# Kernel optimization log

Measured on AMD Instinct MI355X. Metric: run time of the kernel, lower is better.

The kernel has to match this reference:

```python
import jax, jax.numpy as jnp
import numpy as np

NEG_INF = -1e30
LRELU_SLOPE = 0.01
KEEP_SCALE = 2.0  # 1/(1-p) with p=0.5


def mixed_act(x, tid):
    # x: [B, H], tid: [H] int type ids
    # 0 relu, 1 tanh, 2 sig, 3 'smin'->Softmax, 4 'smax'->Softmin, 5 gelu, 6 lrelu
    relu = jnp.maximum(x, 0.0)
    tanh = jnp.tanh(x)
    sig = jax.nn.sigmoid(x)
    gelu = jax.nn.gelu(x, approximate=False)
    lrelu = jnp.where(x >= 0, x, LRELU_SLOPE * x)
    # softmax/softmin restricted to the columns of that type (matches x[:, idx] gather)
    smin = jax.nn.softmax(jnp.where(tid == 3, x, NEG_INF), axis=1)
    smax = jax.nn.softmax(jnp.where(tid == 4, -x, NEG_INF), axis=1)
    return jnp.select(
        [tid == 0, tid == 1, tid == 2, tid == 3, tid == 4, tid == 5, tid == 6],
        [relu, tanh, sig, smin, smax, gelu, lrelu],
    )


def setup_inputs() -> dict:
    key = jax.random.key(0)
    ks = jax.random.split(key, 16)
    B, D_IN, H, C = 32768, 784, 1024, 10
    s_in, s_h = 1.0 / np.sqrt(D_IN), 1.0 / np.sqrt(H)
    inp = {
        "x": jax.random.normal(ks[0], (B, D_IN), jnp.float32),
        "W0": jax.random.normal(ks[1], (H, D_IN), jnp.float32) * s_in,
        "b0": jax.random.normal(ks[2], (H,), jnp.float32) * s_in,
        "W1": jax.random.normal(ks[3], (H, H), jnp.float32) * s_h,
        "b1": jax.random.normal(ks[4], (H,), jnp.float32) * s_h,
        "W2": jax.random.normal(ks[5], (H, H), jnp.float32) * s_h,
        "b2": jax.random.normal(ks[6], (H,), jnp.float32) * s_h,
        "W3": jax.random.normal(ks[7], (C, H), jnp.float32) * s_h,
        "b3": jax.random.normal(ks[8], (C,), jnp.float32) * s_h,
        "mask1": jax.random.bernoulli(ks[9], 0.5, (B, H)).astype(jnp.float32),
        "mask2": jax.random.bernoulli(ks[10], 0.5, (B, H)).astype(jnp.float32),
        "mask3": jax.random.bernoulli(ks[11], 0.5, (B, H)).astype(jnp.float32),
        "type_ids": jax.random.randint(ks[12], (3, H), 0, 7, jnp.int32),
    }
    return inp


def reference(x, W0, b0, W1, b1, W2, b2, W3, b3, mask1, mask2, mask3, type_ids):
    h = mixed_act(x @ W0.T + b0, type_ids[0])
    h = mixed_act((h * mask1 * KEEP_SCALE) @ W1.T + b1, type_ids[1])
    h = mixed_act((h * mask2 * KEEP_SCALE) @ W2.T + b2, type_ids[2])
    logits = (h * mask3 * KEEP_SCALE) @ W3.T + b3
    out = jax.nn.log_softmax(logits, axis=1)
    return (out, mask1, mask2, mask3)
```

## Files before the change

### kernel.cpp

```cpp
#include <hip/hip_runtime.h>
#include <hip/hip_bf16.h>
#include <cstdint>
#include <cstddef>

typedef __bf16 bf16_t;
typedef bf16_t bf16x8 __attribute__((ext_vector_type(8)));
typedef bf16_t bf16x4 __attribute__((ext_vector_type(4)));
typedef float f32x4 __attribute__((ext_vector_type(4)));

#define NEG_BIG (-1e30f)

__global__ __launch_bounds__(256) void convert_pad(const float* __restrict__ src,
                                                   bf16_t* __restrict__ dst,
                                                   int incols, int outcols) {
    const int row = blockIdx.x;
    const float* s = src + (size_t)row * incols;
    bf16_t* d = dst + (size_t)row * outcols;
    const int n4 = outcols >> 2;
    for (int c = threadIdx.x; c < n4; c += blockDim.x) {
        const int col = c << 2;
        float4 v;
        if (col < incols) v = *(const float4*)(s + col);
        else              v = make_float4(0.f, 0.f, 0.f, 0.f);
        bf16x4 o;
        o[0] = (bf16_t)v.x; o[1] = (bf16_t)v.y; o[2] = (bf16_t)v.z; o[3] = (bf16_t)v.w;
        *(bf16x4*)(d + col) = o;
    }
}

#define BM 128
#define BN 128
#define BK 32

__global__ __launch_bounds__(256) void gemm_bt(const bf16_t* __restrict__ A,
                                               const bf16_t* __restrict__ W,
                                               const float* __restrict__ bias,
                                               bf16_t* __restrict__ Z,
                                               int K, int N) {
    __shared__ __align__(16) bf16_t As[BM * BK];
    __shared__ __align__(16) bf16_t Bs[BN * BK];
    const int tid  = threadIdx.x;
    const int wid  = tid >> 6;
    const int lane = tid & 63;

    const int bid = (int)blockIdx.x;
    const int cpx = (int)gridDim.x >> 3;
    const int swz = (bid & 7) * cpx + (bid >> 3);
    const int nbn = N >> 7;
    const int n0 = (swz % nbn) * BN;
    const int m0 = (swz / nbn) * BM;

    const int wm = (wid >> 1) * 64;
    const int wn = (wid & 1) * 64;

    f32x4 acc[4][4] = {};

    const int srow0 = wid * 32 + (lane >> 2);
    const int scol  = (lane & 3) * 8;

    const bf16_t* Aptr0 = A + (size_t)(m0 + srow0) * K + scol;
    const bf16_t* Aptr1 = A + (size_t)(m0 + srow0 + 16) * K + scol;
    const bf16_t* Wptr0 = W + (size_t)(n0 + srow0) * K + scol;
    const bf16_t* Wptr1 = W + (size_t)(n0 + srow0 + 16) * K + scol;

    bf16_t* AsB0 = As + (wid * 2 + 0) * 512;
    bf16_t* AsB1 = As + (wid * 2 + 1) * 512;
    bf16_t* BsB0 = Bs + (wid * 2 + 0) * 512;
    bf16_t* BsB1 = Bs + (wid * 2 + 1) * 512;

    for (int k0 = 0; k0 < K; k0 += BK) {
        __syncthreads();
        __builtin_amdgcn_global_load_lds((const __attribute__((address_space(1))) void*)(Aptr0 + k0),
                                         (__attribute__((address_space(3))) void*)AsB0, 16, 0, 0);
        __builtin_amdgcn_global_load_lds((const __attribute__((address_space(1))) void*)(Aptr1 + k0),
                                         (__attribute__((address_space(3))) void*)AsB1, 16, 0, 0);
        __builtin_amdgcn_global_load_lds((const __attribute__((address_space(1))) void*)(Wptr0 + k0),
                                         (__attribute__((address_space(3))) void*)BsB0, 16, 0, 0);
        __builtin_amdgcn_global_load_lds((const __attribute__((address_space(1))) void*)(Wptr1 + k0),
                                         (__attribute__((address_space(3))) void*)BsB1, 16, 0, 0);
        __syncthreads();

        const int arow = wm + (lane & 15);
        const int brow = wn + (lane & 15);
        const int koff = (lane >> 4) * 8;
        bf16x8 af[4], bfr[4];
        #pragma unroll
        for (int i = 0; i < 4; ++i)
            af[i] = *(const bf16x8*)(As + (arow + i * 16) * BK + koff);
        #pragma unroll
        for (int j = 0; j < 4; ++j)
            bfr[j] = *(const bf16x8*)(Bs + (brow + j * 16) * BK + koff);
        #pragma unroll
        for (int i = 0; i < 4; ++i)
            #pragma unroll
            for (int j = 0; j < 4; ++j)
                acc[i][j] = __builtin_amdgcn_mfma_f32_16x16x32_bf16(af[i], bfr[j], acc[i][j], 0, 0, 0);
    }

    const int cq = lane >> 4;
    const int cl = lane & 15;
    #pragma unroll
    for (int j = 0; j < 4; ++j) {
        const int col = n0 + wn + j * 16 + cl;
        const float bj = bias[col];
        #pragma unroll
        for (int i = 0; i < 4; ++i) {
            const int row = m0 + wm + i * 16 + cq * 4;
            #pragma unroll
            for (int r = 0; r < 4; ++r)
                Z[(size_t)(row + r) * N + col] = (bf16_t)(acc[i][j][r] + bj);
        }
    }
}

__global__ __launch_bounds__(256) void act_kernel(const bf16_t* __restrict__ Z,
                                                  const float* __restrict__ mask,
                                                  const int* __restrict__ tids,
                                                  bf16_t* __restrict__ H,
                                                  float* __restrict__ mask_out) {
    const int wid  = threadIdx.x >> 6;
    const int lane = threadIdx.x & 63;
    const int row  = (int)blockIdx.x * 4 + wid;
    const size_t rb = (size_t)row * 1024;

    float z[16], e[16];
    int   ty[16];
    float4 mk[4];
    float s3 = 0.f, s4 = 0.f;

    #pragma unroll
    for (int q = 0; q < 4; ++q) {
        const int c0 = (q * 64 + lane) * 4;
        const bf16x4 z4 = *(const bf16x4*)(Z + rb + c0);
        const int4   t4 = *(const int4*)(tids + c0);
        mk[q] = *(const float4*)(mask + rb + c0);
        const int tt[4] = {t4.x, t4.y, t4.z, t4.w};
        #pragma unroll
        for (int j = 0; j < 4; ++j) {
            const int i = q * 4 + j;
            const float zz = (float)z4[j];
            z[i] = zz; ty[i] = tt[j];
            const float az = fabsf(zz);
            const float arg = (tt[j] == 1) ? -2.f * az
                            : (tt[j] == 2) ? -az
                            : (tt[j] == 3) ? zz
                            : (tt[j] == 4) ? -zz : 0.f;
            const float ee = __expf(arg);
            e[i] = ee;
            s3 += (tt[j] == 3) ? ee : 0.f;
            s4 += (tt[j] == 4) ? ee : 0.f;
        }
    }
    #pragma unroll
    for (int off = 32; off > 0; off >>= 1) {
        s3 += __shfl_xor(s3, off);
        s4 += __shfl_xor(s4, off);
    }
    const float inv3 = 1.f / s3;
    const float inv4 = 1.f / s4;

    #pragma unroll
    for (int q = 0; q < 4; ++q) {
        const int c0 = (q * 64 + lane) * 4;
        const float mm[4] = {mk[q].x, mk[q].y, mk[q].z, mk[q].w};
        bf16x4 h4;
        #pragma unroll
        for (int j = 0; j < 4; ++j) {
            const int i = q * 4 + j;
            const float zz = z[i], ee = e[i];
            const int tt = ty[i];
            const float r1pe = __builtin_amdgcn_rcpf(1.f + ee);
            const float tha = (1.f - ee) * r1pe;
            const float tnh = (zz >= 0.f) ? tha : -tha;
            const float sg  = ((zz >= 0.f) ? 1.f : ee) * r1pe;
            const float gel = 0.5f * zz * (1.f + erff(zz * 0.70710678f));
            const float a = (tt == 0) ? fmaxf(zz, 0.f)
                          : (tt == 1) ? tnh
                          : (tt == 2) ? sg
                          : (tt == 3) ? ee * inv3
                          : (tt == 4) ? ee * inv4
                          : (tt == 5) ? gel
                          : fmaxf(zz, 0.01f * zz);
            h4[j] = (bf16_t)(a * mm[j] * 2.0f);
        }
        *(bf16x4*)(H + rb + c0) = h4;
        *(float4*)(mask_out + rb + c0) = mk[q];
    }
}

__global__ __launch_bounds__(256) void act_final(const bf16_t* __restrict__ Z,
                                                 const float* __restrict__ mask,
                                                 const int* __restrict__ tids,
                                                 const bf16_t* __restrict__ W3b,
                                                 const float* __restrict__ b3,
                                                 float* __restrict__ mask_out,
                                                 float* __restrict__ out) {
    __shared__ __align__(16) bf16_t Ws[10 * 1024];
    #pragma unroll
    for (int i = threadIdx.x * 8; i < 10240; i += 2048)
        *(bf16x8*)(Ws + i) = *(const bf16x8*)(W3b + i);
    __syncthreads();

    const int wid  = threadIdx.x >> 6;
    const int lane = threadIdx.x & 63;
    const int row  = (int)blockIdx.x * 4 + wid;
    const size_t rb = (size_t)row * 1024;

    float z[16], e[16];
    float4 mk[4];
    float s3 = 0.f, s4 = 0.f;

    #pragma unroll
    for (int q = 0; q < 4; ++q) {
        const int c0 = (q * 64 + lane) * 4;
        const bf16x4 z4 = *(const bf16x4*)(Z + rb + c0);
        const int4   t4 = *(const int4*)(tids + c0);
        mk[q] = *(const float4*)(mask + rb + c0);
        const int tt[4] = {t4.x, t4.y, t4.z, t4.w};
        #pragma unroll
        for (int j = 0; j < 4; ++j) {
            const int i = q * 4 + j;
            const float zz = (float)z4[j];
            z[i] = zz;
            const float az = fabsf(zz);
            const float arg = (tt[j] == 1) ? -2.f * az
                            : (tt[j] == 2) ? -az
                            : (tt[j] == 3) ? zz
                            : (tt[j] == 4) ? -zz : 0.f;
            const float ee = __expf(arg);
            e[i] = ee;
            s3 += (tt[j] == 3) ? ee : 0.f;
            s4 += (tt[j] == 4) ? ee : 0.f;
        }
    }
    #pragma unroll
    for (int off = 32; off > 0; off >>= 1) {
        s3 += __shfl_xor(s3, off);
        s4 += __shfl_xor(s4, off);
    }
    const float inv3 = 1.f / s3;
    const float inv4 = 1.f / s4;

    float acc[10];
    #pragma unroll
    for (int n = 0; n < 10; ++n) acc[n] = 0.f;

    #pragma unroll
    for (int q = 0; q < 4; ++q) {
        const int c0 = (q * 64 + lane) * 4;
        const int4 t4 = *(const int4*)(tids + c0);
        const int tt4[4] = {t4.x, t4.y, t4.z, t4.w};
        const float mm[4] = {mk[q].x, mk[q].y, mk[q].z, mk[q].w};
        float h[4];
        #pragma unroll
        for (int j = 0; j < 4; ++j) {
            const int i = q * 4 + j;
            const float zz = z[i], ee = e[i];
            const int tt = tt4[j];
            const float r1pe = __builtin_amdgcn_rcpf(1.f + ee);
            const float tha = (1.f - ee) * r1pe;
            const float tnh = (zz >= 0.f) ? tha : -tha;
            const float sg  = ((zz >= 0.f) ? 1.f : ee) * r1pe;
            const float gel = 0.5f * zz * (1.f + erff(zz * 0.70710678f));
            const float a = (tt == 0) ? fmaxf(zz, 0.f)
                          : (tt == 1) ? tnh
                          : (tt == 2) ? sg
                          : (tt == 3) ? ee * inv3
                          : (tt == 4) ? ee * inv4
                          : (tt == 5) ? gel
                          : fmaxf(zz, 0.01f * zz);
            h[j] = a * mm[j] * 2.0f;
        }
        *(float4*)(mask_out + rb + c0) = mk[q];
        #pragma unroll
        for (int n = 0; n < 10; ++n) {
            const bf16x4 w4 = *(const bf16x4*)(Ws + n * 1024 + c0);
            acc[n] += h[0] * (float)w4[0] + h[1] * (float)w4[1]
                    + h[2] * (float)w4[2] + h[3] * (float)w4[3];
        }
    }

    #pragma unroll
    for (int n = 0; n < 10; ++n)
        #pragma unroll
        for (int off = 32; off > 0; off >>= 1)
            acc[n] += __shfl_xor(acc[n], off);

    if (lane == 0) {
        float lg[10]; float mx = -1e30f;
        #pragma unroll
        for (int n = 0; n < 10; ++n) { lg[n] = acc[n] + b3[n]; mx = fmaxf(mx, lg[n]); }
        float se = 0.f;
        #pragma unroll
        for (int n = 0; n < 10; ++n) se += __expf(lg[n] - mx);
        const float lse = logf(se) + mx;
        #pragma unroll
        for (int n = 0; n < 10; ++n) out[(size_t)row * 10 + n] = lg[n] - lse;
    }
}

extern "C" void kernel_launch(void* const* d_in, const int* in_sizes, int n_in,
                              void* d_out, int out_size, void* d_ws, size_t ws_size,
                              hipStream_t stream) {
    (void)in_sizes; (void)n_in; (void)out_size; (void)ws_size;
    const float* x     = (const float*)d_in[0];
    const float* W0    = (const float*)d_in[1];
    const float* b0    = (const float*)d_in[2];
    const float* W1    = (const float*)d_in[3];
    const float* b1    = (const float*)d_in[4];
    const float* W2    = (const float*)d_in[5];
    const float* b2    = (const float*)d_in[6];
    const float* W3    = (const float*)d_in[7];
    const float* b3    = (const float*)d_in[8];
    const float* mask1 = (const float*)d_in[9];
    const float* mask2 = (const float*)d_in[10];
    const float* mask3 = (const float*)d_in[11];
    const int*   tids  = (const int*)d_in[12];

    float* out = (float*)d_out;
    float* mo1 = out + 327680;
    float* mo2 = mo1 + 33554432;
    float* mo3 = mo2 + 33554432;

    char* ws = (char*)d_ws;
    bf16_t* xb  = (bf16_t*)ws;  ws += (size_t)32768 * 800 * 2;
    bf16_t* W0b = (bf16_t*)ws;  ws += (size_t)1024 * 800 * 2;
    bf16_t* W1b = (bf16_t*)ws;  ws += (size_t)1024 * 1024 * 2;
    bf16_t* W2b = (bf16_t*)ws;  ws += (size_t)1024 * 1024 * 2;
    bf16_t* W3b = (bf16_t*)ws;  ws += (size_t)16 * 1024 * 2;
    bf16_t* Zb  = (bf16_t*)ws;  ws += (size_t)32768 * 1024 * 2;
    bf16_t* hb  = (bf16_t*)ws;  ws += (size_t)32768 * 1024 * 2;

    convert_pad<<<32768, 256, 0, stream>>>(x,  xb,  784, 800);
    convert_pad<<<1024,  256, 0, stream>>>(W0, W0b, 784, 800);
    convert_pad<<<1024,  256, 0, stream>>>(W1, W1b, 1024, 1024);
    convert_pad<<<1024,  256, 0, stream>>>(W2, W2b, 1024, 1024);
    convert_pad<<<10,    256, 0, stream>>>(W3, W3b, 1024, 1024);

    gemm_bt<<<2048, 256, 0, stream>>>(xb, W0b, b0, Zb, 800, 1024);
    act_kernel<<<8192, 256, 0, stream>>>(Zb, mask1, tids, hb, mo1);
    gemm_bt<<<2048, 256, 0, stream>>>(hb, W1b, b1, Zb, 1024, 1024);
    act_kernel<<<8192, 256, 0, stream>>>(Zb, mask2, tids + 1024, hb, mo2);
    gemm_bt<<<2048, 256, 0, stream>>>(hb, W2b, b2, Zb, 1024, 1024);
    act_final<<<8192, 256, 0, stream>>>(Zb, mask3, tids + 2048, W3b, b3, mo3, out);
}
```

Before: 1.203 ms.

## Double GEMM K-tile with XOR-swizzled LDS and widen activation kernel vectors

```diff
diff --git a/kernel.cpp b/kernel.cpp
--- a/kernel.cpp
+++ b/kernel.cpp
@@ -30,7 +30,7 @@
 
 #define BM 128
 #define BN 128
-#define BK 32
+#define BK 64
 
 __global__ __launch_bounds__(256) void gemm_bt(const bf16_t* __restrict__ A,
                                                const bf16_t* __restrict__ W,
@@ -55,46 +55,51 @@
 
     f32x4 acc[4][4] = {};
 
-    const int srow0 = wid * 32 + (lane >> 2);
-    const int scol  = (lane & 3) * 8;
-
-    const bf16_t* Aptr0 = A + (size_t)(m0 + srow0) * K + scol;
-    const bf16_t* Aptr1 = A + (size_t)(m0 + srow0 + 16) * K + scol;
-    const bf16_t* Wptr0 = W + (size_t)(n0 + srow0) * K + scol;
-    const bf16_t* Wptr1 = W + (size_t)(n0 + srow0 + 16) * K + scol;
-
-    bf16_t* AsB0 = As + (wid * 2 + 0) * 512;
-    bf16_t* AsB1 = As + (wid * 2 + 1) * 512;
-    bf16_t* BsB0 = Bs + (wid * 2 + 0) * 512;
-    bf16_t* BsB1 = Bs + (wid * 2 + 1) * 512;
+    const int srow = wid * 32 + (lane >> 3);
+    const int scol = (((lane & 7) ^ ((lane >> 3) & 7)) * 8);
+    const bf16_t* Ab = A + (size_t)(m0 + srow) * K + scol;
+    const bf16_t* Wb = W + (size_t)(n0 + srow) * K + scol;
+    bf16_t* AsW = As + wid * 2048;
+    bf16_t* BsW = Bs + wid * 2048;
+    const size_t rstep = (size_t)8 * K;
 
     for (int k0 = 0; k0 < K; k0 += BK) {
         __syncthreads();
-        __builtin_amdgcn_global_load_lds((const __attribute__((address_space(1))) void*)(Aptr0 + k0),
-                                         (__attribute__((address_space(3))) void*)AsB0, 16, 0, 0);
-        __builtin_amdgcn_global_load_lds((const __attribute__((address_space(1))) void*)(Aptr1 + k0),
-                                         (__attribute__((address_space(3))) void*)AsB1, 16, 0, 0);
-        __builtin_amdgcn_global_load_lds((const __attribute__((address_space(1))) void*)(Wptr0 + k0),
-                                         (__attribute__((address_space(3))) void*)BsB0, 16, 0, 0);
-        __builtin_amdgcn_global_load_lds((const __attribute__((address_space(1))) void*)(Wptr1 + k0),
-                                         (__attribute__((address_space(3))) void*)BsB1, 16, 0, 0);
+        #pragma unroll
+        for (int t = 0; t < 4; ++t)
+            __builtin_amdgcn_global_load_lds(
+                (const __attribute__((address_space(1))) void*)(Ab + k0 + t * rstep),
+                (__attribute__((address_space(3))) void*)(AsW + t * 512), 16, 0, 0);
+        #pragma unroll
+        for (int t = 0; t < 4; ++t)
+            __builtin_amdgcn_global_load_lds(
+                (const __attribute__((address_space(1))) void*)(Wb + k0 + t * rstep),
+                (__attribute__((address_space(3))) void*)(BsW + t * 512), 16, 0, 0);
         __syncthreads();
 
         const int arow = wm + (lane & 15);
         const int brow = wn + (lane & 15);
-        const int koff = (lane >> 4) * 8;
-        bf16x8 af[4], bfr[4];
-        #pragma unroll
-        for (int i = 0; i < 4; ++i)
-            af[i] = *(const bf16x8*)(As + (arow + i * 16) * BK + koff);
-        #pragma unroll
-        for (int j = 0; j < 4; ++j)
-            bfr[j] = *(const bf16x8*)(Bs + (brow + j * 16) * BK + koff);
-        #pragma unroll
-        for (int i = 0; i < 4; ++i)
+        const int qb   = (lane >> 4) * 16;
+        const int rxa  = (arow & 7) << 4;
+        const int rxb  = (brow & 7) << 4;
+        const char* Ac = (const char*)As;
+        const char* Bc = (const char*)Bs;
+
+        #pragma unroll
+        for (int kh = 0; kh < 2; ++kh) {
+            bf16x8 af[4], bfr[4];
+            #pragma unroll
+            for (int i = 0; i < 4; ++i)
+                af[i] = *(const bf16x8*)(Ac + ((((arow + i * 16) << 7) + qb + kh * 64) ^ rxa));
             #pragma unroll
             for (int j = 0; j < 4; ++j)
-                acc[i][j] = __builtin_amdgcn_mfma_f32_16x16x32_bf16(af[i], bfr[j], acc[i][j], 0, 0, 0);
+                bfr[j] = *(const bf16x8*)(Bc + ((((brow + j * 16) << 7) + qb + kh * 64) ^ rxb));
+            #pragma unroll
+            for (int i = 0; i < 4; ++i)
+                #pragma unroll
+                for (int j = 0; j < 4; ++j)
+                    acc[i][j] = __builtin_amdgcn_mfma_f32_16x16x32_bf16(af[i], bfr[j], acc[i][j], 0, 0, 0);
+        }
     }
 
     const int cq = lane >> 4;
@@ -123,68 +128,72 @@
     const int row  = (int)blockIdx.x * 4 + wid;
     const size_t rb = (size_t)row * 1024;
 
-    float z[16], e[16];
-    int   ty[16];
-    float4 mk[4];
+    float p[16], mk[16];
+    uint32_t m3 = 0, m4 = 0;
     float s3 = 0.f, s4 = 0.f;
 
     #pragma unroll
-    for (int q = 0; q < 4; ++q) {
-        const int c0 = (q * 64 + lane) * 4;
-        const bf16x4 z4 = *(const bf16x4*)(Z + rb + c0);
-        const int4   t4 = *(const int4*)(tids + c0);
-        mk[q] = *(const float4*)(mask + rb + c0);
-        const int tt[4] = {t4.x, t4.y, t4.z, t4.w};
-        #pragma unroll
-        for (int j = 0; j < 4; ++j) {
-            const int i = q * 4 + j;
-            const float zz = (float)z4[j];
-            z[i] = zz; ty[i] = tt[j];
+    for (int q = 0; q < 2; ++q) {
+        const int c0 = (q * 64 + lane) * 8;
+        const bf16x8 z8 = *(const bf16x8*)(Z + rb + c0);
+        const int4   ta = *(const int4*)(tids + c0);
+        const int4   tb = *(const int4*)(tids + c0 + 4);
+        const float4 ma = *(const float4*)(mask + rb + c0);
+        const float4 mb = *(const float4*)(mask + rb + c0 + 4);
+        const int   tt8[8] = {ta.x, ta.y, ta.z, ta.w, tb.x, tb.y, tb.z, tb.w};
+        const float mm8[8] = {ma.x, ma.y, ma.z, ma.w, mb.x, mb.y, mb.z, mb.w};
+        #pragma unroll
+        for (int j = 0; j < 8; ++j) {
+            const int i = q * 8 + j;
+            const float zz = (float)z8[j];
+            const int tt = tt8[j];
+            mk[i] = mm8[j];
             const float az = fabsf(zz);
-            const float arg = (tt[j] == 1) ? -2.f * az
-                            : (tt[j] == 2) ? -az
-                            : (tt[j] == 3) ? zz
-                            : (tt[j] == 4) ? -zz : 0.f;
+            const float arg = (tt == 1) ? -2.f * az
+                            : (tt == 2) ? -az
+                            : (tt == 3) ? zz
+                            : (tt == 4) ? -zz : 0.f;
             const float ee = __expf(arg);
-            e[i] = ee;
-            s3 += (tt[j] == 3) ? ee : 0.f;
-            s4 += (tt[j] == 4) ? ee : 0.f;
-        }
-    }
-    #pragma unroll
-    for (int off = 32; off > 0; off >>= 1) {
-        s3 += __shfl_xor(s3, off);
-        s4 += __shfl_xor(s4, off);
-    }
-    const float inv3 = 1.f / s3;
-    const float inv4 = 1.f / s4;
-
-    #pragma unroll
-    for (int q = 0; q < 4; ++q) {
-        const int c0 = (q * 64 + lane) * 4;
-        const float mm[4] = {mk[q].x, mk[q].y, mk[q].z, mk[q].w};
-        bf16x4 h4;
-        #pragma unroll
-        for (int j = 0; j < 4; ++j) {
-            const int i = q * 4 + j;
-            const float zz = z[i], ee = e[i];
-            const int tt = ty[i];
             const float r1pe = __builtin_amdgcn_rcpf(1.f + ee);
             const float tha = (1.f - ee) * r1pe;
             const float tnh = (zz >= 0.f) ? tha : -tha;
             const float sg  = ((zz >= 0.f) ? 1.f : ee) * r1pe;
             const float gel = 0.5f * zz * (1.f + erff(zz * 0.70710678f));
-            const float a = (tt == 0) ? fmaxf(zz, 0.f)
-                          : (tt == 1) ? tnh
-                          : (tt == 2) ? sg
-                          : (tt == 3) ? ee * inv3
-                          : (tt == 4) ? ee * inv4
-                          : (tt == 5) ? gel
-                          : fmaxf(zz, 0.01f * zz);
-            h4[j] = (bf16_t)(a * mm[j] * 2.0f);
-        }
-        *(bf16x4*)(H + rb + c0) = h4;
-        *(float4*)(mask_out + rb + c0) = mk[q];
+            const float pre = (tt == 0) ? fmaxf(zz, 0.f)
+                            : (tt == 1) ? tnh
+                            : (tt == 2) ? sg
+                            : (tt == 3) ? ee
+                            : (tt == 4) ? ee
+                            : (tt == 5) ? gel
+                            : fmaxf(zz, 0.01f * zz);
+            p[i] = pre;
+            m3 |= (uint32_t)(tt == 3) << i;
+            m4 |= (uint32_t)(tt == 4) << i;
+            s3 += (tt == 3) ? ee : 0.f;
+            s4 += (tt == 4) ? ee : 0.f;
+        }
+        *(float4*)(mask_out + rb + c0)     = ma;
+        *(float4*)(mask_out + rb + c0 + 4) = mb;
+    }
+    #pragma unroll
+    for (int off = 32; off > 0; off >>= 1) {
+        s3 += __shfl_xor(s3, off);
+        s4 += __shfl_xor(s4, off);
+    }
+    const float inv3 = 1.f / s3;
+    const float inv4 = 1.f / s4;
+
+    #pragma unroll
+    for (int q = 0; q < 2; ++q) {
+        const int c0 = (q * 64 + lane) * 8;
+        bf16x8 h8;
+        #pragma unroll
+        for (int j = 0; j < 8; ++j) {
+            const int i = q * 8 + j;
+            const float sc = ((m3 >> i) & 1) ? inv3 : ((m4 >> i) & 1) ? inv4 : 1.f;
+            h8[j] = (bf16_t)(p[i] * sc * mk[i] * 2.0f);
+        }
+        *(bf16x8*)(H + rb + c0) = h8;
     }
 }
 
@@ -206,77 +215,82 @@
     const int row  = (int)blockIdx.x * 4 + wid;
     const size_t rb = (size_t)row * 1024;
 
-    float z[16], e[16];
-    float4 mk[4];
+    float p[16], mk[16];
+    uint32_t m3 = 0, m4 = 0;
     float s3 = 0.f, s4 = 0.f;
 
     #pragma unroll
-    for (int q = 0; q < 4; ++q) {
-        const int c0 = (q * 64 + lane) * 4;
-        const bf16x4 z4 = *(const bf16x4*)(Z + rb + c0);
-        const int4   t4 = *(const int4*)(tids + c0);
-        mk[q] = *(const float4*)(mask + rb + c0);
-        const int tt[4] = {t4.x, t4.y, t4.z, t4.w};
-        #pragma unroll
-        for (int j = 0; j < 4; ++j) {
-            const int i = q * 4 + j;
-            const float zz = (float)z4[j];
-            z[i] = zz;
+    for (int q = 0; q < 2; ++q) {
+        const int c0 = (q * 64 + lane) * 8;
+        const bf16x8 z8 = *(const bf16x8*)(Z + rb + c0);
+        const int4   ta = *(const int4*)(tids + c0);
+        const int4   tb = *(const int4*)(tids + c0 + 4);
+        const float4 ma = *(const float4*)(mask + rb + c0);
+        const float4 mb = *(const float4*)(mask + rb + c0 + 4);
+        const int   tt8[8] = {ta.x, ta.y, ta.z, ta.w, tb.x, tb.y, tb.z, tb.w};
+        const float mm8[8] = {ma.x, ma.y, ma.z, ma.w, mb.x, mb.y, mb.z, mb.w};
+        #pragma unroll
+        for (int j = 0; j < 8; ++j) {
+            const int i = q * 8 + j;
+            const float zz = (float)z8[j];
+            const int tt = tt8[j];
+            mk[i] = mm8[j];
             const float az = fabsf(zz);
-            const float arg = (tt[j] == 1) ? -2.f * az
-                            : (tt[j] == 2) ? -az
-                            : (tt[j] == 3) ? zz
-                            : (tt[j] == 4) ? -zz : 0.f;
+            const float arg = (tt == 1) ? -2.f * az
+                            : (tt == 2) ? -az
+                            : (tt == 3) ? zz
+                            : (tt == 4) ? -zz : 0.f;
             const float ee = __expf(arg);
-            e[i] = ee;
-            s3 += (tt[j] == 3) ? ee : 0.f;
-            s4 += (tt[j] == 4) ? ee : 0.f;
-        }
-    }
-    #pragma unroll
-    for (int off = 32; off > 0; off >>= 1) {
-        s3 += __shfl_xor(s3, off);
-        s4 += __shfl_xor(s4, off);
-    }
-    const float inv3 = 1.f / s3;
-    const float inv4 = 1.f / s4;
-
-    float acc[10];
-    #pragma unroll
-    for (int n = 0; n < 10; ++n) acc[n] = 0.f;
-
-    #pragma unroll
-    for (int q = 0; q < 4; ++q) {
-        const int c0 = (q * 64 + lane) * 4;
-        const int4 t4 = *(const int4*)(tids + c0);
-        const int tt4[4] = {t4.x, t4.y, t4.z, t4.w};
-        const float mm[4] = {mk[q].x, mk[q].y, mk[q].z, mk[q].w};
-        float h[4];
-        #pragma unroll
-        for (int j = 0; j < 4; ++j) {
-            const int i = q * 4 + j;
-            const float zz = z[i], ee = e[i];
-            const int tt = tt4[j];
             const float r1pe = __builtin_amdgcn_rcpf(1.f + ee);
             const float tha = (1.f - ee) * r1pe;
             const float tnh = (zz >= 0.f) ? tha : -tha;
             const float sg  = ((zz >= 0.f) ? 1.f : ee) * r1pe;
             const float gel = 0.5f * zz * (1.f + erff(zz * 0.70710678f));
-            const float a = (tt == 0) ? fmaxf(zz, 0.f)
-                          : (tt == 1) ? tnh
-                          : (tt == 2) ? sg
-                          : (tt == 3) ? ee * inv3
-                          : (tt == 4) ? ee * inv4
-                          : (tt == 5) ? gel
-                          : fmaxf(zz, 0.01f * zz);
-            h[j] = a * mm[j] * 2.0f;
-        }
-        *(float4*)(mask_out + rb + c0) = mk[q];
+            const float pre = (tt == 0) ? fmaxf(zz, 0.f)
+                            : (tt == 1) ? tnh
+                            : (tt == 2) ? sg
+                            : (tt == 3) ? ee
+                            : (tt == 4) ? ee
+                            : (tt == 5) ? gel
+                            : fmaxf(zz, 0.01f * zz);
+            p[i] = pre;
+            m3 |= (uint32_t)(tt == 3) << i;
+            m4 |= (uint32_t)(tt == 4) << i;
+            s3 += (tt == 3) ? ee : 0.f;
+            s4 += (tt == 4) ? ee : 0.f;
+        }
+        *(float4*)(mask_out + rb + c0)     = ma;
+        *(float4*)(mask_out + rb + c0 + 4) = mb;
+    }
+    #pragma unroll
+    for (int off = 32; off > 0; off >>= 1) {
+        s3 += __shfl_xor(s3, off);
+        s4 += __shfl_xor(s4, off);
+    }
+    const float inv3 = 1.f / s3;
+    const float inv4 = 1.f / s4;
+
+    float acc[10];
+    #pragma unroll
+    for (int n = 0; n < 10; ++n) acc[n] = 0.f;
+
+    #pragma unroll
+    for (int q = 0; q < 2; ++q) {
+        const int c0 = (q * 64 + lane) * 8;
+        float h[8];
+        #pragma unroll
+        for (int j = 0; j < 8; ++j) {
+            const int i = q * 8 + j;
+            const float sc = ((m3 >> i) & 1) ? inv3 : ((m4 >> i) & 1) ? inv4 : 1.f;
+            h[j] = p[i] * sc * mk[i] * 2.0f;
+        }
         #pragma unroll
         for (int n = 0; n < 10; ++n) {
-            const bf16x4 w4 = *(const bf16x4*)(Ws + n * 1024 + c0);
-            acc[n] += h[0] * (float)w4[0] + h[1] * (float)w4[1]
-                    + h[2] * (float)w4[2] + h[3] * (float)w4[3];
+            const bf16x8 w8 = *(const bf16x8*)(Ws + n * 1024 + c0);
+            float d = 0.f;
+            #pragma unroll
+            for (int j = 0; j < 8; ++j) d += h[j] * (float)w8[j];
+            acc[n] += d;
         }
     }
 
@@ -323,21 +337,21 @@
     float* mo3 = mo2 + 33554432;
 
     char* ws = (char*)d_ws;
-    bf16_t* xb  = (bf16_t*)ws;  ws += (size_t)32768 * 800 * 2;
-    bf16_t* W0b = (bf16_t*)ws;  ws += (size_t)1024 * 800 * 2;
+    bf16_t* xb  = (bf16_t*)ws;  ws += (size_t)32768 * 832 * 2;
+    bf16_t* W0b = (bf16_t*)ws;  ws += (size_t)1024 * 832 * 2;
     bf16_t* W1b = (bf16_t*)ws;  ws += (size_t)1024 * 1024 * 2;
     bf16_t* W2b = (bf16_t*)ws;  ws += (size_t)1024 * 1024 * 2;
     bf16_t* W3b = (bf16_t*)ws;  ws += (size_t)16 * 1024 * 2;
     bf16_t* Zb  = (bf16_t*)ws;  ws += (size_t)32768 * 1024 * 2;
     bf16_t* hb  = (bf16_t*)ws;  ws += (size_t)32768 * 1024 * 2;
 
-    convert_pad<<<32768, 256, 0, stream>>>(x,  xb,  784, 800);
-    convert_pad<<<1024,  256, 0, stream>>>(W0, W0b, 784, 800);
+    convert_pad<<<32768, 256, 0, stream>>>(x,  xb,  784, 832);
+    convert_pad<<<1024,  256, 0, stream>>>(W0, W0b, 784, 832);
     convert_pad<<<1024,  256, 0, stream>>>(W1, W1b, 1024, 1024);
     convert_pad<<<1024,  256, 0, stream>>>(W2, W2b, 1024, 1024);
     convert_pad<<<10,    256, 0, stream>>>(W3, W3b, 1024, 1024);
 
-    gemm_bt<<<2048, 256, 0, stream>>>(xb, W0b, b0, Zb, 800, 1024);
+    gemm_bt<<<2048, 256, 0, stream>>>(xb, W0b, b0, Zb, 832, 1024);
     act_kernel<<<8192, 256, 0, stream>>>(Zb, mask1, tids, hb, mo1);
     gemm_bt<<<2048, 256, 0, stream>>>(hb, W1b, b1, Zb, 1024, 1024);
     act_kernel<<<8192, 256, 0, stream>>>(Zb, mask2, tids + 1024, hb, mo2);
```

Result: faster. 1.131 ms (-6.0%).
